# Kernel optimization log

Measured on AMD Instinct MI355X. Metric: run time of the kernel, lower is better.

The kernel has to match this reference:

```python
import jax, jax.numpy as jnp
import numpy as np

N = 8192        # num nodes
F_IN = 128      # input feature dim
H = 2           # num heads
DH = 64         # per-head output dim (output_dim // num_heads)
NEG = -1e9


def setup_inputs() -> dict:
    key = jax.random.key(0)
    k1, k2, k3, k4, k5 = jax.random.split(key, 5)
    node_features = jax.random.normal(k1, (N, F_IN), dtype=jnp.float32)
    # sparse binary adjacency (~avg degree 32) + self loops, stored dense as float
    adj = (jax.random.uniform(k2, (N, N)) < (32.0 / N)).astype(jnp.float32)
    adj = jnp.maximum(adj, jnp.eye(N, dtype=jnp.float32))
    W = jax.random.normal(k3, (H, F_IN, DH), dtype=jnp.float32) * 0.1
    a_self = jax.random.normal(k4, (H, DH), dtype=jnp.float32) * 0.1
    a_neigh = jax.random.normal(k5, (H, DH), dtype=jnp.float32) * 0.1
    bias = jnp.zeros((H * DH,), dtype=jnp.float32)
    return {"node_features": node_features, "adj_matrix": adj,
            "W": W, "a_self": a_self, "a_neigh": a_neigh, "bias": bias}


def reference(node_features, adj_matrix, W, a_self, a_neigh, bias):
    # transformed features per head: [H, N, DH]
    h = jnp.einsum('nf,hfd->hnd', node_features, W)
    s_self = jnp.einsum('hnd,hd->hn', h, a_self)    # [H, N]
    s_neigh = jnp.einsum('hnd,hd->hn', h, a_neigh)  # [H, N]
    # additive broadcast scores: score[h,i,j] = s_self[h,i] + s_neigh[h,j]
    scores = s_self[:, :, None] + s_neigh[:, None, :]          # [H, N, N]
    scores = scores + (1.0 - adj_matrix)[None] * NEG            # mask non-edges
    attn = jax.nn.softmax(scores, axis=-1)                      # row softmax
    ctx = jnp.einsum('hij,hjd->hid', attn, h)                   # [H, N, DH]
    out = jnp.transpose(ctx, (1, 0, 2)).reshape(node_features.shape[0], -1)  # concat heads
    out = out + bias
    return jax.nn.elu(out)
```

## Files before the change

### kernel.cpp

```cpp
#include <hip/hip_runtime.h>
#include <math.h>

#define N_NODES 8192
#define F_IN 128
#define DH 64
#define H_HEADS 2
#define MAX_E 256

__global__ __launch_bounds__(128) void gat_transform(
    const float* __restrict__ X, const float* __restrict__ W,
    const float* __restrict__ a_neigh, float* __restrict__ hbuf,
    float* __restrict__ sneigh) {
  const int n = blockIdx.x;
  const int t = threadIdx.x;
  const int head = t >> 6;
  const int d = t & 63;

  __shared__ float xs[F_IN];
  xs[t] = X[(size_t)n * F_IN + t];
  __syncthreads();

  const float* Wc = W + (size_t)head * F_IN * DH + d;
  float acc = 0.f;
#pragma unroll
  for (int f = 0; f < F_IN; ++f) acc = fmaf(xs[f], Wc[(size_t)f * DH], acc);

  hbuf[((size_t)head * N_NODES + n) * DH + d] = acc;

  float p = acc * a_neigh[head * DH + d];
#pragma unroll
  for (int off = 32; off > 0; off >>= 1) p += __shfl_xor(p, off, 64);
  if (d == 0) sneigh[head * N_NODES + n] = p;
}

__global__ __launch_bounds__(256) void gat_attn(
    const float* __restrict__ adj, const float* __restrict__ hbuf,
    const float* __restrict__ sneigh, const float* __restrict__ bias,
    float* __restrict__ out) {
  const int i = blockIdx.x;
  const int t = threadIdx.x;

  __shared__ int eidx[MAX_E];
  __shared__ float wexp[H_HEADS][MAX_E];
  __shared__ int ecnt;
  __shared__ float red0[256], red1[256];

  if (t == 0) ecnt = 0;
  __syncthreads();

  const float4* row = (const float4*)(adj + (size_t)i * N_NODES);
#pragma unroll
  for (int b = t; b < N_NODES / 4; b += 256) {
    float4 v = row[b];
    int j0 = b * 4;
    if (v.x > 0.5f) { int e = atomicAdd(&ecnt, 1); if (e < MAX_E) eidx[e] = j0; }
    if (v.y > 0.5f) { int e = atomicAdd(&ecnt, 1); if (e < MAX_E) eidx[e] = j0 + 1; }
    if (v.z > 0.5f) { int e = atomicAdd(&ecnt, 1); if (e < MAX_E) eidx[e] = j0 + 2; }
    if (v.w > 0.5f) { int e = atomicAdd(&ecnt, 1); if (e < MAX_E) eidx[e] = j0 + 3; }
  }
  __syncthreads();
  const int deg = min(ecnt, MAX_E);

  float m0 = -1e30f, m1 = -1e30f;
  for (int e = t; e < deg; e += 256) {
    int j = eidx[e];
    m0 = fmaxf(m0, sneigh[j]);
    m1 = fmaxf(m1, sneigh[N_NODES + j]);
  }
  red0[t] = m0; red1[t] = m1;
  __syncthreads();
#pragma unroll
  for (int s = 128; s > 0; s >>= 1) {
    if (t < s) {
      red0[t] = fmaxf(red0[t], red0[t + s]);
      red1[t] = fmaxf(red1[t], red1[t + s]);
    }
    __syncthreads();
  }
  const float M0 = red0[0], M1 = red1[0];
  __syncthreads();

  float z0 = 0.f, z1 = 0.f;
  for (int e = t; e < deg; e += 256) {
    int j = eidx[e];
    float w0 = __expf(sneigh[j] - M0);
    float w1 = __expf(sneigh[N_NODES + j] - M1);
    wexp[0][e] = w0; wexp[1][e] = w1;
    z0 += w0; z1 += w1;
  }
  red0[t] = z0; red1[t] = z1;
  __syncthreads();
#pragma unroll
  for (int s = 128; s > 0; s >>= 1) {
    if (t < s) {
      red0[t] += red0[t + s];
      red1[t] += red1[t + s];
    }
    __syncthreads();
  }
  const float Z0 = red0[0], Z1 = red1[0];

  if (t < 128) {
    const int head = t >> 6;
    const int dd = t & 63;
    const float* hb = hbuf + (size_t)head * N_NODES * DH + dd;
    const float* wl = wexp[head];
    float ctx = 0.f;
    for (int e = 0; e < deg; ++e) {
      ctx = fmaf(wl[e], hb[(size_t)eidx[e] * DH], ctx);
    }
    float val = ctx / (head ? Z1 : Z0) + bias[t];
    out[(size_t)i * (H_HEADS * DH) + t] = val > 0.f ? val : expm1f(val);
  }
}

extern "C" void kernel_launch(void* const* d_in, const int* in_sizes, int n_in,
                              void* d_out, int out_size, void* d_ws, size_t ws_size,
                              hipStream_t stream) {
  const float* X       = (const float*)d_in[0];
  const float* adj     = (const float*)d_in[1];
  const float* W       = (const float*)d_in[2];
  const float* a_neigh = (const float*)d_in[4];
  const float* bias    = (const float*)d_in[5];
  float* out = (float*)d_out;

  float* hbuf   = (float*)d_ws;
  float* sneigh = hbuf + (size_t)H_HEADS * N_NODES * DH;

  gat_transform<<<N_NODES, 128, 0, stream>>>(X, W, a_neigh, hbuf, sneigh);
  gat_attn<<<N_NODES, 256, 0, stream>>>(adj, hbuf, sneigh, bias, out);
}
```

Baseline: 392.1 us.

## Tile node transform, use wave-level softmax, split aggregation across all threads

```diff
diff --git a/kernel.cpp b/kernel.cpp
--- a/kernel.cpp
+++ b/kernel.cpp
@@ -5,32 +5,48 @@
 #define F_IN 128
 #define DH 64
 #define H_HEADS 2
-#define MAX_E 256
+#define MAX_E 192
+#define TILE 8
 
-__global__ __launch_bounds__(128) void gat_transform(
+__global__ __launch_bounds__(256) void gat_transform(
     const float* __restrict__ X, const float* __restrict__ W,
     const float* __restrict__ a_neigh, float* __restrict__ hbuf,
     float* __restrict__ sneigh) {
-  const int n = blockIdx.x;
+  const int node0 = blockIdx.x * TILE;
   const int t = threadIdx.x;
-  const int head = t >> 6;
-  const int d = t & 63;
+  const int c = t & 127;
+  const int grp = t >> 7;
+  const int head = c >> 6;
+  const int d = c & 63;
 
-  __shared__ float xs[F_IN];
-  xs[t] = X[(size_t)n * F_IN + t];
+  __shared__ float xs[TILE][F_IN];
+  {
+    const float4* src = (const float4*)(X + (size_t)node0 * F_IN);
+    float4* dst = (float4*)&xs[0][0];
+    dst[t] = src[t];
+  }
   __syncthreads();
 
   const float* Wc = W + (size_t)head * F_IN * DH + d;
-  float acc = 0.f;
+  float acc[TILE / 2] = {0.f, 0.f, 0.f, 0.f};
+  const int nb = grp * (TILE / 2);
+#pragma unroll 16
+  for (int f = 0; f < F_IN; ++f) {
+    const float w = Wc[(size_t)f * DH];
 #pragma unroll
-  for (int f = 0; f < F_IN; ++f) acc = fmaf(xs[f], Wc[(size_t)f * DH], acc);
+    for (int k = 0; k < TILE / 2; ++k) acc[k] = fmaf(xs[nb + k][f], w, acc[k]);
+  }
 
-  hbuf[((size_t)head * N_NODES + n) * DH + d] = acc;
-
-  float p = acc * a_neigh[head * DH + d];
+  const float av = a_neigh[c];
 #pragma unroll
-  for (int off = 32; off > 0; off >>= 1) p += __shfl_xor(p, off, 64);
-  if (d == 0) sneigh[head * N_NODES + n] = p;
+  for (int k = 0; k < TILE / 2; ++k) {
+    const int n = node0 + nb + k;
+    hbuf[((size_t)head * N_NODES + n) * DH + d] = acc[k];
+    float p = acc[k] * av;
+#pragma unroll
+    for (int off = 32; off > 0; off >>= 1) p += __shfl_xor(p, off, 64);
+    if (d == 0) sneigh[head * N_NODES + n] = p;
+  }
 }
 
 __global__ __launch_bounds__(256) void gat_attn(
@@ -42,8 +58,8 @@
 
   __shared__ int eidx[MAX_E];
   __shared__ float wexp[H_HEADS][MAX_E];
+  __shared__ float partial[2][128];
   __shared__ int ecnt;
-  __shared__ float red0[256], red1[256];
 
   if (t == 0) ecnt = 0;
   __syncthreads();
@@ -61,55 +77,53 @@
   __syncthreads();
   const int deg = min(ecnt, MAX_E);
 
-  float m0 = -1e30f, m1 = -1e30f;
-  for (int e = t; e < deg; e += 256) {
-    int j = eidx[e];
-    m0 = fmaxf(m0, sneigh[j]);
-    m1 = fmaxf(m1, sneigh[N_NODES + j]);
+  if (t < 64) {
+    float m0 = -1e30f, m1 = -1e30f;
+    for (int e = t; e < deg; e += 64) {
+      int j = eidx[e];
+      m0 = fmaxf(m0, sneigh[j]);
+      m1 = fmaxf(m1, sneigh[N_NODES + j]);
+    }
+#pragma unroll
+    for (int off = 32; off > 0; off >>= 1) {
+      m0 = fmaxf(m0, __shfl_xor(m0, off, 64));
+      m1 = fmaxf(m1, __shfl_xor(m1, off, 64));
+    }
+    float z0 = 0.f, z1 = 0.f;
+    for (int e = t; e < deg; e += 64) {
+      int j = eidx[e];
+      float w0 = __expf(sneigh[j] - m0);
+      float w1 = __expf(sneigh[N_NODES + j] - m1);
+      wexp[0][e] = w0; wexp[1][e] = w1;
+      z0 += w0; z1 += w1;
+    }
+#pragma unroll
+    for (int off = 32; off > 0; off >>= 1) {
+      z0 += __shfl_xor(z0, off, 64);
+      z1 += __shfl_xor(z1, off, 64);
+    }
+    const float r0 = 1.f / z0, r1 = 1.f / z1;
+    for (int e = t; e < deg; e += 64) {
+      wexp[0][e] *= r0;
+      wexp[1][e] *= r1;
+    }
   }
-  red0[t] = m0; red1[t] = m1;
-  __syncthreads();
-#pragma unroll
-  for (int s = 128; s > 0; s >>= 1) {
-    if (t < s) {
-      red0[t] = fmaxf(red0[t], red0[t + s]);
-      red1[t] = fmaxf(red1[t], red1[t + s]);
-    }
-    __syncthreads();
-  }
-  const float M0 = red0[0], M1 = red1[0];
   __syncthreads();
 
-  float z0 = 0.f, z1 = 0.f;
-  for (int e = t; e < deg; e += 256) {
-    int j = eidx[e];
-    float w0 = __expf(sneigh[j] - M0);
-    float w1 = __expf(sneigh[N_NODES + j] - M1);
-    wexp[0][e] = w0; wexp[1][e] = w1;
-    z0 += w0; z1 += w1;
-  }
-  red0[t] = z0; red1[t] = z1;
+  const int c = t & 127;
+  const int half = t >> 7;
+  const int head = c >> 6;
+  const int d = c & 63;
+  const float* hb = hbuf + (size_t)head * N_NODES * DH + d;
+  const float* wl = wexp[head];
+  float ctx = 0.f;
+  for (int e = half; e < deg; e += 2)
+    ctx = fmaf(wl[e], hb[(size_t)eidx[e] * DH], ctx);
+  partial[half][c] = ctx;
   __syncthreads();
-#pragma unroll
-  for (int s = 128; s > 0; s >>= 1) {
-    if (t < s) {
-      red0[t] += red0[t + s];
-      red1[t] += red1[t + s];
-    }
-    __syncthreads();
-  }
-  const float Z0 = red0[0], Z1 = red1[0];
 
   if (t < 128) {
-    const int head = t >> 6;
-    const int dd = t & 63;
-    const float* hb = hbuf + (size_t)head * N_NODES * DH + dd;
-    const float* wl = wexp[head];
-    float ctx = 0.f;
-    for (int e = 0; e < deg; ++e) {
-      ctx = fmaf(wl[e], hb[(size_t)eidx[e] * DH], ctx);
-    }
-    float val = ctx / (head ? Z1 : Z0) + bias[t];
+    float val = partial[0][t] + partial[1][t] + bias[t];
     out[(size_t)i * (H_HEADS * DH) + t] = val > 0.f ? val : expm1f(val);
   }
 }
@@ -127,6 +141,6 @@
   float* hbuf   = (float*)d_ws;
   float* sneigh = hbuf + (size_t)H_HEADS * N_NODES * DH;
 
-  gat_transform<<<N_NODES, 128, 0, stream>>>(X, W, a_neigh, hbuf, sneigh);
+  gat_transform<<<N_NODES / TILE, 256, 0, stream>>>(X, W, a_neigh, hbuf, sneigh);
   gat_attn<<<N_NODES, 256, 0, stream>>>(adj, hbuf, sneigh, bias, out);
 }
```

Measured after the change: 396.2 us. No clear change (+1.0%).
